# Kernel tuning notes

Hardware: AMD Instinct MI355X
Metric: run time of the kernel (lower is better)

The kernel has to match this reference:

```python
import jax, jax.numpy as jnp
import numpy as np

N = 100000
E = 1600000
DIN = 165
DH = 128


def setup_inputs() -> dict:
    key = jax.random.key(0)
    ks = jax.random.split(key, 10)
    def nrm(k, shape, scale=0.1):
        return jax.random.normal(k, shape, dtype=jnp.float32) * scale
    x = jax.random.normal(ks[0], (N, DIN), dtype=jnp.float32)
    edge_index = jax.random.randint(ks[1], (2, E), 0, N, dtype=jnp.int64)
    return dict(
        x=x,
        edge_index=edge_index,
        fb_w1=nrm(ks[2], (DIN, DIN // 2)),
        fb_w2=nrm(ks[3], (DIN // 2, DIN)),
        sage_wl=nrm(ks[4], (DIN, DH)),
        sage_bl=jnp.zeros((DH,), jnp.float32),
        sage_wr=nrm(ks[5], (DIN, DH)),
        gat_w=nrm(ks[6], (DH, DH // 2)),
        gat_att_src=nrm(ks[7], (DH // 2,)),
        gat_att_dst=nrm(ks[8], (DH // 2,)),
        gat_b=jnp.zeros((DH // 2,), jnp.float32),
        cheb_w=nrm(ks[9], (DH // 2, 1)),
        cheb_b=jnp.zeros((1,), jnp.float32),
    )


def _segment_softmax(logits, seg, num_segments):
    mx = jax.ops.segment_max(logits, seg, num_segments=num_segments)
    e = jnp.exp(logits - mx[seg])
    s = jax.ops.segment_sum(e, seg, num_segments=num_segments)
    return e / (s[seg] + 1e-16)


def reference(x, edge_index, fb_w1, fb_w2, sage_wl, sage_bl, sage_wr,
              gat_w, gat_att_src, gat_att_dst, gat_b, cheb_w, cheb_b):
    n = x.shape[0]
    src, dst = edge_index[0], edge_index[1]

    # FeatureBooster: scatter over batch=arange(n) is identity for max and sum,
    # so max_result == sum_result == x and y = sigmoid(mlp(x) + mlp(x)).
    m = jnp.maximum(x @ fb_w1, 0.0) @ fb_w2
    x = x * jax.nn.sigmoid(m + m)

    # SAGEConv (mean aggregation): out = lin_l(mean_agg(x_src -> dst)) + lin_r(x)
    agg = jax.ops.segment_sum(x[src], dst, num_segments=n)  # [n, DIN]
    cnt = jax.ops.segment_sum(jnp.ones((src.shape[0],), x.dtype), dst, num_segments=n)
    agg = agg / jnp.maximum(cnt, 1.0)[:, None]
    x = agg @ sage_wl + sage_bl + x @ sage_wr
    x = jnp.maximum(x, 0.0)  # relu; dropout is identity in eval mode

    # GATConv (heads=1) with default add_self_loops=True
    ar = jnp.arange(n, dtype=src.dtype)
    si = jnp.concatenate([src, ar])
    di = jnp.concatenate([dst, ar])
    h = x @ gat_w                      # [n, 64]
    a_s = h @ gat_att_src              # [n]
    a_d = h @ gat_att_dst              # [n]
    e = a_s[si] + a_d[di]
    e = jnp.where(e > 0, e, 0.2 * e)   # leaky_relu slope 0.2
    alpha = _segment_softmax(e, di, n)
    x = jax.ops.segment_sum(h[si] * alpha[:, None], di, num_segments=n) + gat_b
    x = jnp.maximum(x, 0.0)

    # ChebConv with K=1: T_0(x) = x, so it's a plain linear layer.
    x = x @ cheb_w + cheb_b
    return jax.nn.sigmoid(x)
```

## Files before the change

kernel.cpp:

```cpp
#include <hip/hip_runtime.h>
#include <hip/hip_bf16.h>

#define N_NODES 100000
#define N_EDGES 1600000
#define DIN 165
#define DHID 82
#define DH 128
#define DG 64

typedef _Float16 f16;
typedef f16 f16x8 __attribute__((ext_vector_type(8)));
typedef f16 f16x4 __attribute__((ext_vector_type(4)));
typedef f16 f16x2 __attribute__((ext_vector_type(2)));
typedef float f32x4 __attribute__((ext_vector_type(4)));

#define MFMA16(a, b, c) __builtin_amdgcn_mfma_f32_16x16x32_f16(a, b, c, 0, 0, 0)


__global__ __launch_bounds__(256) void rank_xpad_kernel(const float* __restrict__ x,
                                                        f16* __restrict__ Xp,
                                                        const int* __restrict__ dst,
                                                        int* __restrict__ cnt,
                                                        int* __restrict__ rank) {
    int gid = blockIdx.x * 256 + threadIdx.x;
    if (gid < N_EDGES) rank[gid] = atomicAdd(&cnt[dst[gid]], 1);
    int node = gid / 48, g = gid % 48;
    int col0 = g * 4;
    f16x4 o;
#pragma unroll
    for (int j = 0; j < 4; j++) {
        int c = col0 + j;
        o[j] = (f16)((c < DIN) ? x[(long)node * DIN + c] : 0.f);
    }
    *((f16x4*)(Xp + (long)node * 192 + col0)) = o;
}

__global__ __launch_bounds__(1024) void scan1_kernel(const int* __restrict__ cnt,
                                                     int* __restrict__ rowptr,
                                                     int* __restrict__ bsum) {
    __shared__ int wsum[16];
    int tid = threadIdx.x, lane = tid & 63, wid = tid >> 6;
    int i = blockIdx.x * 1024 + tid;
    int v = (i < N_NODES) ? cnt[i] : 0;
    int xv = v;
#pragma unroll
    for (int off = 1; off < 64; off <<= 1) {
        int t = __shfl_up(xv, off);
        if (lane >= off) xv += t;
    }
    if (lane == 63) wsum[wid] = xv;
    __syncthreads();
    if (wid == 0 && lane < 16) {
        int wv = wsum[lane];
#pragma unroll
        for (int off = 1; off < 16; off <<= 1) {
            int t = __shfl_up(wv, off);
            if (lane >= off) wv += t;
        }
        wsum[lane] = wv;
    }
    __syncthreads();
    int off0 = wid ? wsum[wid - 1] : 0;
    if (i < N_NODES) rowptr[i] = off0 + xv - v;
    if (tid == 1023) bsum[blockIdx.x] = off0 + xv;
}

__global__ __launch_bounds__(64) void scan2_kernel(const int* __restrict__ bsum,
                                                   int* __restrict__ boff,
                                                   int* __restrict__ rowptr,
                                                   int nblocks) {
    int lane = threadIdx.x;
    int c = 0;
    for (int base = 0; base < nblocks; base += 64) {
        int idx = base + lane;
        int v = (idx < nblocks) ? bsum[idx] : 0;
        int xv = v;
#pragma unroll
        for (int off = 1; off < 64; off <<= 1) {
            int t = __shfl_up(xv, off);
            if (lane >= off) xv += t;
        }
        if (idx < nblocks) boff[idx] = c + xv - v;
        c += __shfl(xv, 63);
    }
    if (lane == 0) rowptr[N_NODES] = c;
}

__global__ __launch_bounds__(1024) void scan3_kernel(int* __restrict__ rowptr,
                                                     const int* __restrict__ boff) {
    int i = blockIdx.x * 1024 + threadIdx.x;
    if (i < N_NODES) rowptr[i] += boff[blockIdx.x];
}

__global__ __launch_bounds__(256) void h_fill_kernel(const f16* __restrict__ Xp,
                                                     const float* __restrict__ w1,
                                                     f16* __restrict__ H,
                                                     const int* __restrict__ src,
                                                     const int* __restrict__ dst,
                                                     const int* __restrict__ rank,
                                                     const int* __restrict__ rowptr,
                                                     int* __restrict__ esrc) {
    int tid = threadIdx.x, wave = tid >> 6, lane = tid & 63;
    {
        int tg = blockIdx.x * 256 + tid;
        for (int e = tg; e < N_EDGES; e += 384 * 256) {
            int d = dst[e];
            __hip_atomic_store(&esrc[rowptr[d] + rank[e]], src[e],
                               __ATOMIC_RELAXED, __HIP_MEMORY_SCOPE_AGENT);
        }
    }
    int q = lane >> 4, l16 = lane & 15;
    int blk = blockIdx.x;
    int g = (blk >> 3) & 1;
    int chunk = (blk & 7) + 8 * (blk >> 4);
    int nbase = g * 48;
    f16x8 bf[3][6];
#pragma unroll
    for (int nt = 0; nt < 3; nt++) {
        int col = nbase + nt * 16 + l16;
#pragma unroll
        for (int ks = 0; ks < 6; ks++) {
            int kb = ks * 32 + q * 8;
            f16x8 b;
#pragma unroll
            for (int j = 0; j < 8; j++) {
                int k = kb + j;
                b[j] = (f16)((k < DIN && col < DHID) ? w1[k * DHID + col] : 0.f);
            }
            bf[nt][ks] = b;
        }
    }
    for (int mt = chunk * 4 + wave; mt < 6250; mt += 768) {
        const f16* xr = Xp + (long)(mt * 16 + l16) * 192;
        f32x4 acc[3];
#pragma unroll
        for (int nt = 0; nt < 3; nt++) acc[nt] = (f32x4){0.f, 0.f, 0.f, 0.f};
#pragma unroll
        for (int ks = 0; ks < 6; ks++) {
            f16x8 a = *((const f16x8*)(xr + ks * 32 + q * 8));
#pragma unroll
            for (int nt = 0; nt < 3; nt++) acc[nt] = MFMA16(a, bf[nt][ks], acc[nt]);
        }
#pragma unroll
        for (int nt = 0; nt < 3; nt++) {
            int col = nbase + nt * 16 + l16;
#pragma unroll
            for (int r = 0; r < 4; r++) {
                int node = mt * 16 + q * 4 + r;
                H[(long)node * 96 + col] = (f16)fmaxf(acc[nt][r], 0.f);
            }
        }
    }
}

__global__ __launch_bounds__(256) void y_kernel(const f16* __restrict__ Xp,
                                                const f16* __restrict__ H,
                                                const float* __restrict__ w2,
                                                f16* __restrict__ Y) {
    int tid = threadIdx.x, wave = tid >> 6, lane = tid & 63;
    int q = lane >> 4, l16 = lane & 15;
    int blk = blockIdx.x;
    int g = (blk >> 3) & 3;
    int chunk = (blk & 7) + 8 * (blk >> 5);
    int nbase = g * 48;
    f16x8 bf[3][3];
#pragma unroll
    for (int nt = 0; nt < 3; nt++) {
        int col = nbase + nt * 16 + l16;
#pragma unroll
        for (int ks = 0; ks < 3; ks++) {
            int kb = ks * 32 + q * 8;
            f16x8 b;
#pragma unroll
            for (int j = 0; j < 8; j++) {
                int k = kb + j;
                b[j] = (f16)((k < DHID && col < DIN) ? w2[k * DIN + col] : 0.f);
            }
            bf[nt][ks] = b;
        }
    }
    for (int mt = chunk * 4 + wave; mt < 6250; mt += 768) {
        const f16* hr = H + (long)(mt * 16 + l16) * 96;
        f32x4 acc[3];
#pragma unroll
        for (int nt = 0; nt < 3; nt++) acc[nt] = (f32x4){0.f, 0.f, 0.f, 0.f};
#pragma unroll
        for (int ks = 0; ks < 3; ks++) {
            f16x8 a = *((const f16x8*)(hr + ks * 32 + q * 8));
#pragma unroll
            for (int nt = 0; nt < 3; nt++) acc[nt] = MFMA16(a, bf[nt][ks], acc[nt]);
        }
#pragma unroll
        for (int nt = 0; nt < 3; nt++) {
            int col = nbase + nt * 16 + l16;
#pragma unroll
            for (int r = 0; r < 4; r++) {
                int node = mt * 16 + q * 4 + r;
                float gg = 1.f / (1.f + __expf(-2.f * acc[nt][r]));
                float xv = (float)Xp[(long)node * 192 + col];
                Y[(long)node * 192 + col] = (f16)(xv * gg);
            }
        }
    }
}

__global__ __launch_bounds__(256) void sage_lin_kernel(const f16* __restrict__ Y,
                                                       const float* __restrict__ wl,
                                                       const float* __restrict__ wr,
                                                       const float* __restrict__ bl,
                                                       f16* __restrict__ t_l,
                                                       f16* __restrict__ x2) {
    int tid = threadIdx.x, wave = tid >> 6, lane = tid & 63;
    int q = lane >> 4, l16 = lane & 15;
    int blk = blockIdx.x;
    int g = (blk >> 3) & 3;
    int chunk = (blk & 7) + 8 * (blk >> 5);
    bool isR = (g >= 2);
    const float* W = isR ? wr : wl;
    int cbase = (g & 1) * 64;
    f16x8 bf[4][6];
    float blv[4];
#pragma unroll
    for (int nt = 0; nt < 4; nt++) {
        int col = cbase + nt * 16 + l16;
        blv[nt] = isR ? bl[col] : 0.f;
#pragma unroll
        for (int ks = 0; ks < 6; ks++) {
            int kb = ks * 32 + q * 8;
            f16x8 b;
#pragma unroll
            for (int j = 0; j < 8; j++) {
                int k = kb + j;
                b[j] = (f16)((k < DIN) ? W[k * DH + col] : 0.f);
            }
            bf[nt][ks] = b;
        }
    }
    for (int mt = chunk * 4 + wave; mt < 6250; mt += 768) {
        const f16* yrow = Y + (long)(mt * 16 + l16) * 192;
        f32x4 acc[4];
#pragma unroll
        for (int nt = 0; nt < 4; nt++) acc[nt] = (f32x4){0.f, 0.f, 0.f, 0.f};
#pragma unroll
        for (int ks = 0; ks < 6; ks++) {
            f16x8 a = *((const f16x8*)(yrow + ks * 32 + q * 8));
#pragma unroll
            for (int nt = 0; nt < 4; nt++) acc[nt] = MFMA16(a, bf[nt][ks], acc[nt]);
        }
#pragma unroll
        for (int nt = 0; nt < 4; nt++) {
            int col = cbase + nt * 16 + l16;
#pragma unroll
            for (int r = 0; r < 4; r++) {
                int node = mt * 16 + q * 4 + r;
                if (isR)
                    x2[(long)node * DH + col] = (f16)(acc[nt][r] + blv[nt]);
                else
                    t_l[(long)node * DH + col] = (f16)acc[nt][r];
            }
        }
    }
}

__global__ __launch_bounds__(256) void sage_agg_kernel(const f16* __restrict__ t_l,
                                                       const int* __restrict__ rowptr,
                                                       const int* __restrict__ esrc,
                                                       f16* __restrict__ x2) {
    int wid = threadIdx.x >> 6, lane = threadIdx.x & 63;
    int i = blockIdx.x * 4 + wid;
    int r0 = rowptr[i], r1 = rowptr[i + 1];
    int quarter = lane >> 4, fq = lane & 15;
    float acc[8];
#pragma unroll
    for (int k = 0; k < 8; k++) acc[k] = 0.f;
    for (int e0 = r0; e0 < r1; e0 += 64) {
        int cnt = min(64, r1 - e0);
        int sn_v = (lane < cnt) ? esrc[e0 + lane] : 0;
        int jmax = (cnt + 3) >> 2;
        for (int j = 0; j < jmax; j++) {
            int idx = 4 * j + quarter;
            int sn = __shfl(sn_v, idx);
            float v = (idx < cnt) ? 1.f : 0.f;
            f16x8 p = *((const f16x8*)(t_l + ((long)sn << 7) + fq * 8));
#pragma unroll
            for (int k = 0; k < 8; k++) acc[k] = fmaf(v, (float)p[k], acc[k]);
        }
    }
#pragma unroll
    for (int k = 0; k < 8; k++) {
        acc[k] += __shfl_xor(acc[k], 16);
        acc[k] += __shfl_xor(acc[k], 32);
    }
    if (quarter == 0) {
        float inv = 1.f / fmaxf((float)(r1 - r0), 1.f);
        f16x8* xp = (f16x8*)(x2 + (long)i * DH + fq * 8);
        f16x8 pre = *xp;
        f16x8 o;
#pragma unroll
        for (int k = 0; k < 8; k++) o[k] = (f16)fmaxf((float)pre[k] + acc[k] * inv, 0.f);
        *xp = o;
    }
}

__global__ __launch_bounds__(256) void gat_h_kernel(const f16* __restrict__ x2,
                                                    const float* __restrict__ gw,
                                                    const float* __restrict__ att_s_w,
                                                    const float* __restrict__ att_d_w,
                                                    f16* __restrict__ h,
                                                    float* __restrict__ a_s,
                                                    float* __restrict__ a_d) {
    int tid = threadIdx.x, wave = tid >> 6, lane = tid & 63;
    int q = lane >> 4, l16 = lane & 15;
    f16x8 bf[4][4];
    float asw[4], adw[4];
#pragma unroll
    for (int nt = 0; nt < 4; nt++) {
        int col = nt * 16 + l16;
        asw[nt] = att_s_w[col];
        adw[nt] = att_d_w[col];
#pragma unroll
        for (int ks = 0; ks < 4; ks++) {
            int kb = ks * 32 + q * 8;
            f16x8 b;
#pragma unroll
            for (int j = 0; j < 8; j++) b[j] = (f16)gw[(kb + j) * DG + col];
            bf[nt][ks] = b;
        }
    }
    int stride = gridDim.x * 4;
    for (int mt = blockIdx.x * 4 + wave; mt < 6250; mt += stride) {
        const f16* xr = x2 + (long)(mt * 16 + l16) * DH;
        f32x4 acc[4];
#pragma unroll
        for (int nt = 0; nt < 4; nt++) acc[nt] = (f32x4){0.f, 0.f, 0.f, 0.f};
#pragma unroll
        for (int ks = 0; ks < 4; ks++) {
            f16x8 a = *((const f16x8*)(xr + ks * 32 + q * 8));
#pragma unroll
            for (int nt = 0; nt < 4; nt++) acc[nt] = MFMA16(a, bf[nt][ks], acc[nt]);
        }
#pragma unroll
        for (int r = 0; r < 4; r++) {
            int node = mt * 16 + q * 4 + r;
            float vs = 0.f, vd = 0.f;
#pragma unroll
            for (int nt = 0; nt < 4; nt++) {
                float hv = acc[nt][r];
                h[(long)node * DG + nt * 16 + l16] = (f16)hv;
                vs += hv * asw[nt];
                vd += hv * adw[nt];
            }
#pragma unroll
            for (int off = 1; off < 16; off <<= 1) {
                vs += __shfl_xor(vs, off);
                vd += __shfl_xor(vd, off);
            }
            if (l16 == 0) {
                a_s[node] = vs;
                a_d[node] = vd;
            }
        }
    }
}

__device__ __forceinline__ float leaky02(float v) { return v > 0.f ? v : 0.2f * v; }

__global__ __launch_bounds__(256) void gat_agg_kernel(const f16* __restrict__ h,
                                                      const float* __restrict__ a_s,
                                                      const float* __restrict__ a_d,
                                                      const int* __restrict__ rowptr,
                                                      const int* __restrict__ esrc,
                                                      const float* __restrict__ gat_b,
                                                      const float* __restrict__ cheb_w,
                                                      const float* __restrict__ cheb_b,
                                                      float* __restrict__ out) {
    int wid = threadIdx.x >> 6, lane = threadIdx.x & 63;
    int i = blockIdx.x * 4 + wid;
    int r0 = rowptr[i], r1 = rowptr[i + 1];
    int quarter = lane >> 4, fq = lane & 15;
    float adi = a_d[i];
    float acc[4] = {0.f, 0.f, 0.f, 0.f};
    float sv = 0.f;
    for (int e0 = r0; e0 < r1; e0 += 64) {
        int cnt = min(64, r1 - e0);
        int sn_v = (lane < cnt) ? esrc[e0 + lane] : 0;
        float ev = 0.f;
        if (lane < cnt) ev = __expf(leaky02(a_s[sn_v] + adi));
        sv += ev;
        int jmax = (cnt + 3) >> 2;
        for (int j = 0; j < jmax; j++) {
            int idx = 4 * j + quarter;
            int sn = __shfl(sn_v, idx);
            float w = __shfl(ev, idx);
            f16x4 p = *((const f16x4*)(h + ((long)sn << 6) + fq * 4));
#pragma unroll
            for (int k = 0; k < 4; k++) acc[k] = fmaf(w, (float)p[k], acc[k]);
        }
    }
#pragma unroll
    for (int off = 32; off > 0; off >>= 1) sv += __shfl_xor(sv, off);
#pragma unroll
    for (int k = 0; k < 4; k++) {
        acc[k] += __shfl_xor(acc[k], 16);
        acc[k] += __shfl_xor(acc[k], 32);
    }
    if (quarter == 0) {
        float wself = __expf(leaky02(a_s[i] + adi));
        float s = sv + wself;
        f16x4 ph = *((const f16x4*)(h + ((long)i << 6) + fq * 4));
        float4 gb = ((const float4*)gat_b)[fq];
        float4 cw = ((const float4*)cheb_w)[fq];
        float gbv[4] = {gb.x, gb.y, gb.z, gb.w};
        float cwv[4] = {cw.x, cw.y, cw.z, cw.w};
        float inv = 1.f / s;
        float z = 0.f;
#pragma unroll
        for (int k = 0; k < 4; k++) {
            float o = fmaxf(fmaf(wself, (float)ph[k], acc[k]) * inv + gbv[k], 0.f);
            z = fmaf(o, cwv[k], z);
        }
#pragma unroll
        for (int off = 8; off > 0; off >>= 1) z += __shfl_xor(z, off);
        if (fq == 0) out[i] = 1.f / (1.f + __expf(-(z + cheb_b[0])));
    }
}

extern "C" void kernel_launch(void* const* d_in, const int* in_sizes, int n_in,
                              void* d_out, int out_size, void* d_ws, size_t ws_size,
                              hipStream_t stream) {
    const float* x       = (const float*)d_in[0];
    const int*   eidx    = (const int*)d_in[1];
    const float* fb_w1   = (const float*)d_in[2];
    const float* fb_w2   = (const float*)d_in[3];
    const float* sage_wl = (const float*)d_in[4];
    const float* sage_bl = (const float*)d_in[5];
    const float* sage_wr = (const float*)d_in[6];
    const float* gat_w   = (const float*)d_in[7];
    const float* att_src = (const float*)d_in[8];
    const float* att_dst = (const float*)d_in[9];
    const float* gat_b   = (const float*)d_in[10];
    const float* cheb_w  = (const float*)d_in[11];
    const float* cheb_b  = (const float*)d_in[12];

    const int* src = eidx;
    const int* dst = eidx + N_EDGES;

    char* base = (char*)d_ws;
    f16* Xp = (f16*)base;
    f16* H  = (f16*)(base + 38400000);
    f16* Y  = (f16*)(base + 57600000);
    f16* t_l = (f16*)base;
    f16* x2  = (f16*)(base + 25600000);
    f16* h   = Y;
    float* a_s = (float*)(base + 70400000);
    float* a_d = a_s + N_NODES;
    int* rowptr = (int*)(base + 96000000);
    int* cnt  = rowptr + (N_NODES + 1);
    int* esrc = cnt + N_NODES;
    int* rank = esrc + N_EDGES;
    int* bsum = rank + N_EDGES;
    int* boff = bsum + 128;

    const int SCAN_BLOCKS = (N_NODES + 1023) / 1024;
    const size_t WS_USED = 96000000UL
                         + (size_t)(N_NODES + 1 + N_NODES + N_EDGES + N_EDGES + 128 + 128) * 4;

    hipMemsetAsync(d_ws, 0, WS_USED, stream);

    rank_xpad_kernel<<<(N_NODES * 48) / 256, 256, 0, stream>>>(x, Xp, dst, cnt, rank);
    scan1_kernel<<<SCAN_BLOCKS, 1024, 0, stream>>>(cnt, rowptr, bsum);
    scan2_kernel<<<1, 64, 0, stream>>>(bsum, boff, rowptr, SCAN_BLOCKS);
    scan3_kernel<<<SCAN_BLOCKS, 1024, 0, stream>>>(rowptr, boff);
    h_fill_kernel<<<384, 256, 0, stream>>>(Xp, fb_w1, H, src, dst, rank, rowptr, esrc);
    y_kernel<<<768, 256, 0, stream>>>(Xp, H, fb_w2, Y);
    sage_lin_kernel<<<768, 256, 0, stream>>>(Y, sage_wl, sage_wr, sage_bl, t_l, x2);
    sage_agg_kernel<<<N_NODES / 4, 256, 0, stream>>>(t_l, rowptr, esrc, x2);
    gat_h_kernel<<<392, 256, 0, stream>>>(x2, gat_w, att_src, att_dst, h, a_s, a_d);
    gat_agg_kernel<<<N_NODES / 4, 256, 0, stream>>>(h, a_s, a_d, rowptr, esrc, gat_b,
                                                    cheb_w, cheb_b, (float*)d_out);
}
```

Baseline: 498.6 us.

## Spread CSR build across the dense MLP kernels and shrink the memset

```diff
diff --git a/kernel.cpp b/kernel.cpp
--- a/kernel.cpp
+++ b/kernel.cpp
@@ -3,6 +3,7 @@
 
 #define N_NODES 100000
 #define N_EDGES 1600000
+#define EHALF 800000
 #define DIN 165
 #define DHID 82
 #define DH 128
@@ -17,13 +18,9 @@
 #define MFMA16(a, b, c) __builtin_amdgcn_mfma_f32_16x16x32_f16(a, b, c, 0, 0, 0)
 
 
-__global__ __launch_bounds__(256) void rank_xpad_kernel(const float* __restrict__ x,
-                                                        f16* __restrict__ Xp,
-                                                        const int* __restrict__ dst,
-                                                        int* __restrict__ cnt,
-                                                        int* __restrict__ rank) {
+__global__ __launch_bounds__(256) void xpad_kernel(const float* __restrict__ x,
+                                                   f16* __restrict__ Xp) {
     int gid = blockIdx.x * 256 + threadIdx.x;
-    if (gid < N_EDGES) rank[gid] = atomicAdd(&cnt[dst[gid]], 1);
     int node = gid / 48, g = gid % 48;
     int col0 = g * 4;
     f16x4 o;
@@ -95,19 +92,14 @@
 __global__ __launch_bounds__(256) void h_fill_kernel(const f16* __restrict__ Xp,
                                                      const float* __restrict__ w1,
                                                      f16* __restrict__ H,
-                                                     const int* __restrict__ src,
                                                      const int* __restrict__ dst,
-                                                     const int* __restrict__ rank,
-                                                     const int* __restrict__ rowptr,
-                                                     int* __restrict__ esrc) {
+                                                     int* __restrict__ cnt,
+                                                     int* __restrict__ rank) {
     int tid = threadIdx.x, wave = tid >> 6, lane = tid & 63;
     {
         int tg = blockIdx.x * 256 + tid;
-        for (int e = tg; e < N_EDGES; e += 384 * 256) {
-            int d = dst[e];
-            __hip_atomic_store(&esrc[rowptr[d] + rank[e]], src[e],
-                               __ATOMIC_RELAXED, __HIP_MEMORY_SCOPE_AGENT);
-        }
+        for (int e = tg; e < EHALF; e += 384 * 256)
+            rank[e] = atomicAdd(&cnt[dst[e]], 1);
     }
     int q = lane >> 4, l16 = lane & 15;
     int blk = blockIdx.x;
@@ -156,8 +148,16 @@
 __global__ __launch_bounds__(256) void y_kernel(const f16* __restrict__ Xp,
                                                 const f16* __restrict__ H,
                                                 const float* __restrict__ w2,
-                                                f16* __restrict__ Y) {
+                                                f16* __restrict__ Y,
+                                                const int* __restrict__ dst,
+                                                int* __restrict__ cnt,
+                                                int* __restrict__ rank) {
     int tid = threadIdx.x, wave = tid >> 6, lane = tid & 63;
+    {
+        int tg = blockIdx.x * 256 + tid;
+        for (int e = EHALF + tg; e < N_EDGES; e += 768 * 256)
+            rank[e] = atomicAdd(&cnt[dst[e]], 1);
+    }
     int q = lane >> 4, l16 = lane & 15;
     int blk = blockIdx.x;
     int g = (blk >> 3) & 3;
@@ -209,8 +209,21 @@
                                                        const float* __restrict__ wr,
                                                        const float* __restrict__ bl,
                                                        f16* __restrict__ t_l,
-                                                       f16* __restrict__ x2) {
+                                                       f16* __restrict__ x2,
+                                                       const int* __restrict__ src,
+                                                       const int* __restrict__ dst,
+                                                       const int* __restrict__ rank,
+                                                       const int* __restrict__ rowptr,
+                                                       int* __restrict__ esrc) {
     int tid = threadIdx.x, wave = tid >> 6, lane = tid & 63;
+    {
+        int tg = blockIdx.x * 256 + tid;
+        for (int e = tg; e < N_EDGES; e += 768 * 256) {
+            int d = dst[e];
+            __hip_atomic_store(&esrc[rowptr[d] + rank[e]], src[e],
+                               __ATOMIC_RELAXED, __HIP_MEMORY_SCOPE_AGENT);
+        }
+    }
     int q = lane >> 4, l16 = lane & 15;
     int blk = blockIdx.x;
     int g = (blk >> 3) & 3;
@@ -462,18 +475,19 @@
     int* boff = bsum + 128;
 
     const int SCAN_BLOCKS = (N_NODES + 1023) / 1024;
-    const size_t WS_USED = 96000000UL
-                         + (size_t)(N_NODES + 1 + N_NODES + N_EDGES + N_EDGES + 128 + 128) * 4;
-
-    hipMemsetAsync(d_ws, 0, WS_USED, stream);
-
-    rank_xpad_kernel<<<(N_NODES * 48) / 256, 256, 0, stream>>>(x, Xp, dst, cnt, rank);
+
+    const size_t INT_BYTES =
+        (size_t)(N_NODES + 1 + N_NODES + N_EDGES + N_EDGES + 128 + 128) * 4;
+    hipMemsetAsync(rowptr, 0, INT_BYTES, stream);
+
+    xpad_kernel<<<(N_NODES * 48) / 256, 256, 0, stream>>>(x, Xp);
+    h_fill_kernel<<<384, 256, 0, stream>>>(Xp, fb_w1, H, dst, cnt, rank);
+    y_kernel<<<768, 256, 0, stream>>>(Xp, H, fb_w2, Y, dst, cnt, rank);
     scan1_kernel<<<SCAN_BLOCKS, 1024, 0, stream>>>(cnt, rowptr, bsum);
     scan2_kernel<<<1, 64, 0, stream>>>(bsum, boff, rowptr, SCAN_BLOCKS);
     scan3_kernel<<<SCAN_BLOCKS, 1024, 0, stream>>>(rowptr, boff);
-    h_fill_kernel<<<384, 256, 0, stream>>>(Xp, fb_w1, H, src, dst, rank, rowptr, esrc);
-    y_kernel<<<768, 256, 0, stream>>>(Xp, H, fb_w2, Y);
-    sage_lin_kernel<<<768, 256, 0, stream>>>(Y, sage_wl, sage_wr, sage_bl, t_l, x2);
+    sage_lin_kernel<<<768, 256, 0, stream>>>(Y, sage_wl, sage_wr, sage_bl, t_l, x2,
+                                             src, dst, rank, rowptr, esrc);
     sage_agg_kernel<<<N_NODES / 4, 256, 0, stream>>>(t_l, rowptr, esrc, x2);
     gat_h_kernel<<<392, 256, 0, stream>>>(x2, gat_w, att_src, att_dst, h, a_s, a_d);
     gat_agg_kernel<<<N_NODES / 4, 256, 0, stream>>>(h, a_s, a_d, rowptr, esrc, gat_b,
```

Result: faster. 486.8 us (-2.4%).
